# Kernel tuning notes

Hardware: AMD Instinct MI355X
Metric: run time of the kernel (lower is better)

## Reference

```python
import jax, jax.numpy as jnp
import numpy as np

EMBED = 1024
HEADS = 16
HEAD_DIM = EMBED // HEADS


def setup_inputs() -> dict:
    key = jax.random.key(0)
    ks = jax.random.split(key, 12)
    B, S = 2, 2048
    inp = {
        "query": jax.random.normal(ks[0], (B, S, EMBED), dtype=jnp.float32),
        "key": jax.random.normal(ks[1], (B, S, EMBED), dtype=jnp.float32),
        "value": jax.random.normal(ks[2], (B, S, EMBED), dtype=jnp.float32),
        "mask": jnp.ones((B, 1, 1, S), dtype=jnp.int32),
    }
    scale = 1.0 / np.sqrt(EMBED)
    inp["Wq"] = jax.random.normal(ks[3], (EMBED, EMBED), dtype=jnp.float32) * scale
    inp["bq"] = jax.random.normal(ks[4], (EMBED,), dtype=jnp.float32) * 0.01
    inp["Wk"] = jax.random.normal(ks[5], (EMBED, EMBED), dtype=jnp.float32) * scale
    inp["bk"] = jax.random.normal(ks[6], (EMBED,), dtype=jnp.float32) * 0.01
    inp["Wv"] = jax.random.normal(ks[7], (EMBED, EMBED), dtype=jnp.float32) * scale
    inp["bv"] = jax.random.normal(ks[8], (EMBED,), dtype=jnp.float32) * 0.01
    inp["Wo"] = jax.random.normal(ks[9], (EMBED, EMBED), dtype=jnp.float32) * scale
    inp["bo"] = jax.random.normal(ks[10], (EMBED,), dtype=jnp.float32) * 0.01
    return inp


def reference(query, key, value, mask, Wq, bq, Wk, bk, Wv, bv, Wo, bo):
    N, Lq, _ = query.shape
    Lk = key.shape[1]
    # Linear projections (torch Linear: x @ W.T + b)
    q = (query @ Wq.T + bq).reshape(N, Lq, HEADS, HEAD_DIM)
    k = (key @ Wk.T + bk).reshape(N, Lk, HEADS, HEAD_DIM)
    v = (value @ Wv.T + bv).reshape(N, Lk, HEADS, HEAD_DIM)
    # scores: [N, H, Lq, Lk]
    energy = jnp.einsum("nqhd,nkhd->nhqk", q, k)
    energy = jnp.where(mask == 0, jnp.float32(-1e20), energy)
    # NOTE: original scales by sqrt(embedSize), not sqrt(head_dim)
    attn = jax.nn.softmax(energy / jnp.sqrt(jnp.float32(EMBED)), axis=3)
    out = jnp.einsum("nhqv,nvhd->nqhd", attn, v).reshape(N, Lq, EMBED)
    return out @ Wo.T + bo
```

## Files before the change

### kernel.cpp

```cpp
#include <hip/hip_runtime.h>
#include <stdint.h>

typedef unsigned short u16;
typedef __attribute__((ext_vector_type(8))) short short8;
typedef __attribute__((ext_vector_type(4))) short short4v;
typedef __attribute__((ext_vector_type(4))) float floatx4;

#define AS_GLOBAL __attribute__((address_space(1)))
#define AS_LDS    __attribute__((address_space(3)))

#define QSCALE 0.045084220f

__device__ __forceinline__ float bf2f(u16 u) {
  union { unsigned int i; float f; } x; x.i = ((unsigned int)u) << 16; return x.f;
}
__device__ __forceinline__ u16 f2bf(float f) {
  union { float f; unsigned int i; } x; x.f = f;
  unsigned int u = x.i;
  u += 0x7fffu + ((u >> 16) & 1u);
  return (u16)(u >> 16);
}
__device__ __forceinline__ u16 f2bf_fast(float f) {
  union { float f; unsigned int i; } x; x.f = f;
  return (u16)((x.i + 0x8000u) >> 16);
}

__device__ __forceinline__ int probe_is_f32(const void* p) {
  const unsigned int* w = (const unsigned int*)p;
  int cnt = 0;
#pragma unroll
  for (int i = 0; i < 64; ++i) {
    unsigned int lo = w[i] & 0xFFFFu;
    int e = (int)((lo >> 7) & 0xFFu);
    cnt += (e >= 117 && e <= 137) ? 1 : 0;
  }
  return cnt < 32;
}

__device__ __forceinline__ short8 ld8(const void* P, size_t off, int isf32) {
  if (isf32) {
    const float* q = (const float*)P + off;
    float4 x = *(const float4*)q;
    float4 y = *(const float4*)(q + 4);
    short8 r;
    r[0] = (short)f2bf(x.x); r[1] = (short)f2bf(x.y);
    r[2] = (short)f2bf(x.z); r[3] = (short)f2bf(x.w);
    r[4] = (short)f2bf(y.x); r[5] = (short)f2bf(y.y);
    r[6] = (short)f2bf(y.z); r[7] = (short)f2bf(y.w);
    return r;
  }
  return *(const short8*)((const u16*)P + off);
}

__device__ __forceinline__ float ldscalar(const void* P, size_t idx, int isf32) {
  return isf32 ? ((const float*)P)[idx] : bf2f(((const u16*)P)[idx]);
}

__global__ __launch_bounds__(256) void cvt7(
    const void* s0, const void* s1, const void* s2, const void* s3,
    const void* s4, const void* s5, const void* s6,
    u16* d0, u16* d1, u16* d2, u16* d3, u16* d4, u16* d5, u16* d6)
{
  const int z = blockIdx.y;
  const void* src; u16* dst; int n;
  switch (z) {
    case 0: src = s0; dst = d0; n = 4194304; break;
    case 1: src = s1; dst = d1; n = 4194304; break;
    case 2: src = s2; dst = d2; n = 4194304; break;
    case 3: src = s3; dst = d3; n = 1048576; break;
    case 4: src = s4; dst = d4; n = 1048576; break;
    case 5: src = s5; dst = d5; n = 1048576; break;
    default: src = s6; dst = d6; n = 1048576; break;
  }
  const int isf32 = probe_is_f32(src);
  for (int i = blockIdx.x * 256 + threadIdx.x; i * 4 < n; i += gridDim.x * 256) {
    if (isf32) {
      float4 x = ((const float4*)src)[i];
      short4v r;
      r[0] = (short)f2bf(x.x); r[1] = (short)f2bf(x.y);
      r[2] = (short)f2bf(x.z); r[3] = (short)f2bf(x.w);
      *(short4v*)(dst + (size_t)i * 4) = r;
    } else {
      *(short4v*)(dst + (size_t)i * 4) = ((const short4v*)src)[i];
    }
  }
}

__device__ __forceinline__ void gemm_core_bf16(
    const u16* __restrict__ A, const u16* __restrict__ W,
    u16* As, u16* Bs, floatx4 acc[4][4], int m0, int n0, int K, int tid)
{
  const int lane = tid & 63, wv = tid >> 6;
  const int wm = wv >> 1, wn = wv & 1;
  const int g = lane >> 4, ml = lane & 15;
  const int r0 = tid >> 2, kc = (tid & 3) << 3;
  const u16* Ag0 = A + (size_t)(m0 + r0) * K + kc;
  const u16* Ag1 = A + (size_t)(m0 + r0 + 64) * K + kc;
  const u16* Bg0 = W + (size_t)(n0 + r0) * K + kc;
  const u16* Bg1 = W + (size_t)(n0 + r0 + 64) * K + kc;

#define STAGE_QKV(buf_, kt_) do {                                              \
    u16* a0 = As + (buf_) * 4096 + tid * 8;                                    \
    u16* b0 = Bs + (buf_) * 4096 + tid * 8;                                    \
    __builtin_amdgcn_global_load_lds((const AS_GLOBAL unsigned int*)(Ag0 + (kt_)), \
                                     (AS_LDS unsigned int*)a0, 16, 0, 0);      \
    __builtin_amdgcn_global_load_lds((const AS_GLOBAL unsigned int*)(Ag1 + (kt_)), \
                                     (AS_LDS unsigned int*)(a0 + 2048), 16, 0, 0); \
    __builtin_amdgcn_global_load_lds((const AS_GLOBAL unsigned int*)(Bg0 + (kt_)), \
                                     (AS_LDS unsigned int*)b0, 16, 0, 0);      \
    __builtin_amdgcn_global_load_lds((const AS_GLOBAL unsigned int*)(Bg1 + (kt_)), \
                                     (AS_LDS unsigned int*)(b0 + 2048), 16, 0, 0); \
  } while (0)

  STAGE_QKV(0, 0);
  int buf = 0;
#pragma unroll 2
  for (int kt = 0; kt < K; kt += 32) {
    const int nk = (kt + 32 < K) ? (kt + 32) : 0;
    STAGE_QKV(buf ^ 1, nk);
    __asm__ __volatile__("s_waitcnt vmcnt(4)\n\ts_barrier" ::: "memory");
    const u16* Ac = As + buf * 4096;
    const u16* Bc = Bs + buf * 4096;
    short8 af[4], bf[4];
#pragma unroll
    for (int i = 0; i < 4; ++i)
      af[i] = *(const short8*)(Ac + (wm * 64 + i * 16 + ml) * 32 + g * 8);
#pragma unroll
    for (int j = 0; j < 4; ++j)
      bf[j] = *(const short8*)(Bc + (wn * 64 + j * 16 + ml) * 32 + g * 8);
#pragma unroll
    for (int i = 0; i < 4; ++i)
#pragma unroll
      for (int j = 0; j < 4; ++j)
        acc[i][j] = __builtin_amdgcn_mfma_f32_16x16x32_bf16(af[i], bf[j], acc[i][j], 0, 0, 0);
    __asm__ __volatile__("s_waitcnt lgkmcnt(0)\n\ts_barrier" ::: "memory");
    buf ^= 1;
  }
#undef STAGE_QKV
  __asm__ __volatile__("s_waitcnt vmcnt(0)" ::: "memory");
}

__device__ __forceinline__ void gemm_core_cvt(
    const void* __restrict__ A, const void* __restrict__ W, int aF32, int bF32,
    u16* As, u16* Bs, floatx4 acc[4][4], int m0, int n0, int K, int tid)
{
  const int lane = tid & 63, wv = tid >> 6;
  const int wm = wv >> 1, wn = wv & 1;
  const int g = lane >> 4, ml = lane & 15;
  const int r0 = tid >> 2, kc = (tid & 3) << 3;
  const size_t offA0 = (size_t)(m0 + r0) * K + kc;
  const size_t offA1 = (size_t)(m0 + r0 + 64) * K + kc;
  const size_t offB0 = (size_t)(n0 + r0) * K + kc;
  const size_t offB1 = (size_t)(n0 + r0 + 64) * K + kc;
  u16* Al0 = As + tid * 8;  u16* Al1 = As + (tid + 256) * 8;
  u16* Bl0 = Bs + tid * 8;  u16* Bl1 = Bs + (tid + 256) * 8;
  for (int kt = 0; kt < K; kt += 32) {
    short8 a0 = ld8(A, offA0 + kt, aF32);
    short8 a1 = ld8(A, offA1 + kt, aF32);
    short8 b0 = ld8(W, offB0 + kt, bF32);
    short8 b1 = ld8(W, offB1 + kt, bF32);
    *(short8*)Al0 = a0;  *(short8*)Al1 = a1;
    *(short8*)Bl0 = b0;  *(short8*)Bl1 = b1;
    __syncthreads();
    short8 af[4], bf[4];
#pragma unroll
    for (int i = 0; i < 4; ++i)
      af[i] = *(const short8*)(As + (wm * 64 + i * 16 + ml) * 32 + g * 8);
#pragma unroll
    for (int j = 0; j < 4; ++j)
      bf[j] = *(const short8*)(Bs + (wn * 64 + j * 16 + ml) * 32 + g * 8);
#pragma unroll
    for (int i = 0; i < 4; ++i)
#pragma unroll
      for (int j = 0; j < 4; ++j)
        acc[i][j] = __builtin_amdgcn_mfma_f32_16x16x32_bf16(af[i], bf[j], acc[i][j], 0, 0, 0);
    __syncthreads();
  }
}

__device__ __forceinline__ void qkv_epilogue(
    floatx4 acc[4][4], const void* Bi, int cF32, u16* O, int m0, int n0,
    int tid, int z)
{
  const int lane = tid & 63, wv = tid >> 6;
  const int wm = wv >> 1, wn = wv & 1, g = lane >> 4, ml = lane & 15;
  const float sc = (z == 0) ? QSCALE : 1.0f;
#pragma unroll
  for (int j = 0; j < 4; ++j) {
    int gn = n0 + wn * 64 + j * 16 + ml;
    float bvv = ldscalar(Bi, (size_t)gn, cF32);
    int h = gn >> 6, d = gn & 63;
    if (z == 2) {
#pragma unroll
      for (int i = 0; i < 4; ++i) {
        int gm0 = m0 + wm * 64 + i * 16 + g * 4;
        int b = gm0 >> 11, s0 = gm0 & 2047;
        short4v pk;
#pragma unroll
        for (int r = 0; r < 4; ++r) pk[r] = (short)f2bf_fast(acc[i][j][r] + bvv);
        *(short4v*)(O + ((((size_t)b * 16 + h) * 64 + d) * 2048 + s0)) = pk;
      }
    } else {
#pragma unroll
      for (int i = 0; i < 4; ++i)
#pragma unroll
        for (int r = 0; r < 4; ++r) {
          int gm = m0 + wm * 64 + i * 16 + g * 4 + r;
          int b = gm >> 11, s = gm & 2047;
          O[(((size_t)b * 16 + h) * 2048 + s) * 64 + d] =
              f2bf_fast((acc[i][j][r] + bvv) * sc);
        }
    }
  }
}

__global__ __launch_bounds__(256) void qkv_gemm_bf16(
    const u16* __restrict__ Xq, const u16* __restrict__ Xk, const u16* __restrict__ Xv,
    const u16* __restrict__ Wq, const u16* __restrict__ Wk, const u16* __restrict__ Wv,
    const void* __restrict__ Bq, const void* __restrict__ Bk, const void* __restrict__ Bv,
    u16* __restrict__ Oq, u16* __restrict__ Ok, u16* __restrict__ Ov)
{
  __align__(16) __shared__ u16 As[8192];
  __align__(16) __shared__ u16 Bs[8192];
  const int z = blockIdx.z;
  const u16* X = (z == 0) ? Xq : (z == 1) ? Xk : Xv;
  const u16* W = (z == 0) ? Wq : (z == 1) ? Wk : Wv;
  const void* Bi = (z == 0) ? Bq : (z == 1) ? Bk : Bv;
  u16* O = (z == 0) ? Oq : (z == 1) ? Ok : Ov;
  const int tid = threadIdx.x;
  const int m0 = blockIdx.x * 128, n0 = blockIdx.y * 128;
  floatx4 acc[4][4] = {};
  gemm_core_bf16(X, W, As, Bs, acc, m0, n0, 1024, tid);
  const int cF32 = probe_is_f32(Bi);
  qkv_epilogue(acc, Bi, cF32, O, m0, n0, tid, z);
}

__global__ __launch_bounds__(256) void qkv_gemm_cvt(
    const void* __restrict__ Xq, const void* __restrict__ Xk, const void* __restrict__ Xv,
    const void* __restrict__ Wq, const void* __restrict__ Wk, const void* __restrict__ Wv,
    const void* __restrict__ Bq, const void* __restrict__ Bk, const void* __restrict__ Bv,
    u16* __restrict__ Oq, u16* __restrict__ Ok, u16* __restrict__ Ov)
{
  __align__(16) __shared__ u16 As[4096];
  __align__(16) __shared__ u16 Bs[4096];
  const int z = blockIdx.z;
  const void* X  = (z == 0) ? Xq : (z == 1) ? Xk : Xv;
  const void* W  = (z == 0) ? Wq : (z == 1) ? Wk : Wv;
  const void* Bi = (z == 0) ? Bq : (z == 1) ? Bk : Bv;
  u16* O = (z == 0) ? Oq : (z == 1) ? Ok : Ov;
  const int aF32 = probe_is_f32(X);
  const int bF32 = probe_is_f32(W);
  const int cF32 = probe_is_f32(Bi);
  const int tid = threadIdx.x;
  const int m0 = blockIdx.y * 128, n0 = blockIdx.x * 128;
  floatx4 acc[4][4] = {};
  gemm_core_cvt(X, W, aF32, bF32, As, Bs, acc, m0, n0, 1024, tid);
  qkv_epilogue(acc, Bi, cF32, O, m0, n0, tid, z);
}

__global__ __launch_bounds__(256) void out_gemm_bf16(
    const u16* __restrict__ X, const u16* __restrict__ W,
    const void* __restrict__ Bi, float* __restrict__ O)
{
  __align__(16) __shared__ u16 As[8192];
  __align__(16) __shared__ u16 Bs[8192];
  const int tid = threadIdx.x;
  const int m0 = blockIdx.x * 128, n0 = blockIdx.y * 128;
  floatx4 acc[4][4] = {};
  gemm_core_bf16(X, W, As, Bs, acc, m0, n0, 1024, tid);
  const int cF32 = probe_is_f32(Bi);
  const int lane = tid & 63, wv = tid >> 6;
  const int wm = wv >> 1, wn = wv & 1, g = lane >> 4, ml = lane & 15;
#pragma unroll
  for (int j = 0; j < 4; ++j) {
    int gn = n0 + wn * 64 + j * 16 + ml;
    float bvv = ldscalar(Bi, (size_t)gn, cF32);
#pragma unroll
    for (int i = 0; i < 4; ++i)
#pragma unroll
      for (int r = 0; r < 4; ++r) {
        int gm = m0 + wm * 64 + i * 16 + g * 4 + r;
        O[(size_t)gm * 1024 + gn] = acc[i][j][r] + bvv;
      }
  }
}

__global__ __launch_bounds__(256) void out_gemm_cvt(
    const u16* __restrict__ X, const void* __restrict__ W,
    const void* __restrict__ Bi, float* __restrict__ O)
{
  __align__(16) __shared__ u16 As[4096];
  __align__(16) __shared__ u16 Bs[4096];
  const int bF32 = probe_is_f32(W);
  const int cF32 = probe_is_f32(Bi);
  const int tid = threadIdx.x;
  const int m0 = blockIdx.y * 128, n0 = blockIdx.x * 128;
  floatx4 acc[4][4] = {};
  gemm_core_cvt(X, W, 0, bF32, As, Bs, acc, m0, n0, 1024, tid);
  const int lane = tid & 63, wv = tid >> 6;
  const int wm = wv >> 1, wn = wv & 1, g = lane >> 4, ml = lane & 15;
#pragma unroll
  for (int j = 0; j < 4; ++j) {
    int gn = n0 + wn * 64 + j * 16 + ml;
    float bvv = ldscalar(Bi, (size_t)gn, cF32);
#pragma unroll
    for (int i = 0; i < 4; ++i)
#pragma unroll
      for (int r = 0; r < 4; ++r) {
        int gm = m0 + wm * 64 + i * 16 + g * 4 + r;
        O[(size_t)gm * 1024 + gn] = acc[i][j][r] + bvv;
      }
  }
}

__global__ __launch_bounds__(256) void flash_attn(
    const u16* __restrict__ Q, const u16* __restrict__ K, const u16* __restrict__ V,
    const int* __restrict__ Mask, u16* __restrict__ O)
{
  __align__(16) __shared__ u16 Ks[2][4096];
  __align__(16) __shared__ u16 Vt[2][4096];
  __align__(16) __shared__ u16 Ps[4][16 * 72];
  __align__(16) __shared__ int Ms[64];
  __shared__ int Wok[4];

  const int qt2 = blockIdx.x;
  const int bh = blockIdx.y;
  const int b = bh >> 4, h = bh & 15;
  const int tid = threadIdx.x;
  const int lane = tid & 63, wv = tid >> 6;
  const int g = lane >> 4, ml = lane & 15;

  const size_t baseQ  = (((size_t)b * 16 + h) * 2048 + (size_t)qt2 * 128) * 64;
  const size_t baseKV = ((size_t)b * 16 + h) * 2048 * 64;

  {
    int la = 1;
#pragma unroll
    for (int i = 0; i < 8; ++i) la &= Mask[b * 2048 + tid * 8 + i];
    int wall = __all(la != 0);
    if (lane == 0) Wok[wv] = wall;
  }

  short8 qf[2][2];
#pragma unroll
  for (int u = 0; u < 2; ++u)
#pragma unroll
    for (int ks = 0; ks < 2; ++ks)
      qf[u][ks] = *(const short8*)(Q + baseQ +
          (size_t)(u * 64 + wv * 16 + ml) * 64 + ks * 32 + g * 8);

  const u16* kg[2]; const u16* vg[2];
#pragma unroll
  for (int t = 0; t < 2; ++t) {
    int s = tid + t * 256;
    int krow = s >> 3, kch = (s & 7) ^ (krow & 7);
    kg[t] = K + baseKV + (size_t)krow * 64 + kch * 8;
    int vd = s >> 3,  vch = (s & 7) ^ (vd & 7);
    vg[t] = V + baseKV + (size_t)vd * 2048 + vch * 8;
  }

  __syncthreads();
  const bool maskall = Wok[0] && Wok[1] && Wok[2] && Wok[3];

#define STAGE_FA(buf_) do {                                                    \
    u16* kb_ = Ks[buf_] + (size_t)(tid & 448) * 8;                             \
    u16* vb_ = Vt[buf_] + (size_t)(tid & 448) * 8;                             \
    __builtin_amdgcn_global_load_lds((const AS_GLOBAL unsigned int*)kg[0],     \
                                     (AS_LDS unsigned int*)kb_, 16, 0, 0);     \
    __builtin_amdgcn_global_load_lds((const AS_GLOBAL unsigned int*)kg[1],     \
                                     (AS_LDS unsigned int*)(kb_ + 2048), 16, 0, 0); \
    __builtin_amdgcn_global_load_lds((const AS_GLOBAL unsigned int*)vg[0],     \
                                     (AS_LDS unsigned int*)vb_, 16, 0, 0);     \
    __builtin_amdgcn_global_load_lds((const AS_GLOBAL unsigned int*)vg[1],     \
                                     (AS_LDS unsigned int*)(vb_ + 2048), 16, 0, 0); \
    kg[0] += 4096; kg[1] += 4096; vg[0] += 64; vg[1] += 64;                    \
  } while (0)

  floatx4 oacc[2][4] = {};
  float lp[2][4] = {};

  STAGE_FA(0);
  int buf = 0;
  for (int kv0 = 0; kv0 < 2048; kv0 += 64) {
    STAGE_FA(buf ^ 1);
    __asm__ __volatile__("s_waitcnt vmcnt(4)\n\ts_barrier" ::: "memory");
    if (!maskall && tid < 64) Ms[tid] = Mask[b * 2048 + kv0 + tid];
    const u16* Kc = Ks[buf];
    const u16* Vc = Vt[buf];

#pragma unroll
    for (int u = 0; u < 2; ++u) {
      float sv[4][4];
#pragma unroll
      for (int j = 0; j < 4; ++j) {
        floatx4 a = {0.f, 0.f, 0.f, 0.f};
        int row = j * 16 + ml;
#pragma unroll
        for (int ks = 0; ks < 2; ++ks) {
          short8 kb = *(const short8*)(Kc + row * 64 + ((((ks << 2) + g) ^ (row & 7)) << 3));
          a = __builtin_amdgcn_mfma_f32_16x16x32_bf16(qf[u][ks], kb, a, 0, 0, 0);
        }
#pragma unroll
        for (int r = 0; r < 4; ++r) sv[j][r] = a[r];
      }
      if (!maskall) {
        int mok[4];
#pragma unroll
        for (int j = 0; j < 4; ++j) mok[j] = Ms[j * 16 + ml];
#pragma unroll
        for (int j = 0; j < 4; ++j)
#pragma unroll
          for (int r = 0; r < 4; ++r)
            sv[j][r] = (mok[j] == 0) ? -1.0e30f : sv[j][r];
      }
#pragma unroll
      for (int j = 0; j < 4; ++j)
#pragma unroll
        for (int r = 0; r < 4; ++r) {
          float p = __builtin_amdgcn_exp2f(sv[j][r]);
          sv[j][r] = p;
          lp[u][r] += p;
        }
#pragma unroll
      for (int j = 0; j < 4; ++j)
#pragma unroll
        for (int r = 0; r < 4; ++r)
          Ps[wv][(g * 4 + r) * 72 + j * 16 + ml] = f2bf_fast(sv[j][r]);

      __asm__ __volatile__("s_waitcnt lgkmcnt(0)" ::: "memory");

      short8 pa[2];
#pragma unroll
      for (int j2 = 0; j2 < 2; ++j2)
        pa[j2] = *(const short8*)(&Ps[wv][ml * 72 + j2 * 32 + g * 8]);
#pragma unroll
      for (int t = 0; t < 4; ++t)
#pragma unroll
        for (int j2 = 0; j2 < 2; ++j2) {
          short8 vb = *(const short8*)(Vc + (t * 16 + ml) * 64 + ((((j2 << 2) + g) ^ (ml & 7)) << 3));
          oacc[u][t] = __builtin_amdgcn_mfma_f32_16x16x32_bf16(pa[j2], vb, oacc[u][t], 0, 0, 0);
        }
    }
    __asm__ __volatile__("s_waitcnt lgkmcnt(0)\n\ts_barrier" ::: "memory");
    buf ^= 1;
  }
#undef STAGE_FA
  __asm__ __volatile__("s_waitcnt vmcnt(0)" ::: "memory");

#pragma unroll
  for (int u = 0; u < 2; ++u) {
    float inv[4];
#pragma unroll
    for (int r = 0; r < 4; ++r) {
      float l = lp[u][r];
      l += __shfl_xor(l, 1);
      l += __shfl_xor(l, 2);
      l += __shfl_xor(l, 4);
      l += __shfl_xor(l, 8);
      inv[r] = (l > 0.f) ? 1.0f / l : 0.f;
    }
#pragma unroll
    for (int t = 0; t < 4; ++t)
#pragma unroll
      for (int r = 0; r < 4; ++r) {
        int q = qt2 * 128 + u * 64 + wv * 16 + g * 4 + r;
        int d = t * 16 + ml;
        O[((size_t)b * 2048 + q) * 1024 + h * 64 + d] = f2bf_fast(oacc[u][t][r] * inv[r]);
      }
  }
}

extern "C" void kernel_launch(void* const* d_in, const int* in_sizes, int n_in,
                              void* d_out, int out_size, void* d_ws, size_t ws_size,
                              hipStream_t stream) {
  const void* q_in = d_in[0];
  const void* k_in = d_in[1];
  const void* v_in = d_in[2];
  const int* mask = (const int*)d_in[3];
  const void* Wq = d_in[4];  const void* bq = d_in[5];
  const void* Wk = d_in[6];  const void* bk = d_in[7];
  const void* Wv = d_in[8];  const void* bv = d_in[9];
  const void* Wo = d_in[10]; const void* bo = d_in[11];

  const size_t NTOK = (size_t)2 * 2048 * 1024;
  const size_t NW   = (size_t)1024 * 1024;

  if (ws_size >= (size_t)67108864) {
    u16* CXq = (u16*)d_ws;
    u16* CXk = CXq + NTOK;
    u16* CXv = CXk + NTOK;
    u16* CWq = CXv + NTOK;
    u16* CWk = CWq + NW;
    u16* CWv = CWk + NW;
    u16* CWo = CWv + NW;
    u16* Qp  = CWo + NW;
    u16* Kp  = Qp + NTOK;
    u16* Vp  = Kp + NTOK;
    u16* Ao  = Vp + NTOK;

    cvt7<<<dim3(1024, 7), 256, 0, stream>>>(q_in, k_in, v_in, Wq, Wk, Wv, Wo,
                                            CXq, CXk, CXv, CWq, CWk, CWv, CWo);
    qkv_gemm_bf16<<<dim3(32, 8, 3), 256, 0, stream>>>(CXq, CXk, CXv,
                                                      CWq, CWk, CWv,
                                                      bq, bk, bv, Qp, Kp, Vp);
    flash_attn<<<dim3(16, 32), 256, 0, stream>>>(Qp, Kp, Vp, mask, Ao);
    out_gemm_bf16<<<dim3(32, 8), 256, 0, stream>>>(Ao, CWo, bo, (float*)d_out);
  } else {
    u16* Qp = (u16*)d_ws;
    u16* Kp = Qp + NTOK;
    u16* Vp = Kp + NTOK;
    u16* Ao = Vp + NTOK;

    qkv_gemm_cvt<<<dim3(8, 32, 3), 256, 0, stream>>>(q_in, k_in, v_in,
                                                     Wq, Wk, Wv, bq, bk, bv,
                                                     Qp, Kp, Vp);
    flash_attn<<<dim3(16, 32), 256, 0, stream>>>(Qp, Kp, Vp, mask, Ao);
    out_gemm_cvt<<<dim3(8, 32), 256, 0, stream>>>(Ao, Wo, bo, (float*)d_out);
  }
}
```

Measured before the change: 260.0 us.

## Fuse fp32-to-bf16 conversion into register-prefetched GEMM loads, drop separate convert pass

Removes the standalone conversion kernel that wrote bf16 copies of activations and weights to workspace. The GEMMs now load fp32 directly and convert in registers, with the next K-tile prefetched into registers while the current tile is computed. It uses a single LDS buffer and templated dtype paths. This saves a full read-and-write pass over about 28 MB of data and one launch. In exchange, GEMM loads double in width and the async global-to-LDS double buffering is lost.

```diff
diff --git a/kernel.cpp b/kernel.cpp
--- a/kernel.cpp
+++ b/kernel.cpp
@@ -56,126 +56,80 @@
   return isf32 ? ((const float*)P)[idx] : bf2f(((const u16*)P)[idx]);
 }
 
-__global__ __launch_bounds__(256) void cvt7(
-    const void* s0, const void* s1, const void* s2, const void* s3,
-    const void* s4, const void* s5, const void* s6,
-    u16* d0, u16* d1, u16* d2, u16* d3, u16* d4, u16* d5, u16* d6)
-{
-  const int z = blockIdx.y;
-  const void* src; u16* dst; int n;
-  switch (z) {
-    case 0: src = s0; dst = d0; n = 4194304; break;
-    case 1: src = s1; dst = d1; n = 4194304; break;
-    case 2: src = s2; dst = d2; n = 4194304; break;
-    case 3: src = s3; dst = d3; n = 1048576; break;
-    case 4: src = s4; dst = d4; n = 1048576; break;
-    case 5: src = s5; dst = d5; n = 1048576; break;
-    default: src = s6; dst = d6; n = 1048576; break;
-  }
-  const int isf32 = probe_is_f32(src);
-  for (int i = blockIdx.x * 256 + threadIdx.x; i * 4 < n; i += gridDim.x * 256) {
-    if (isf32) {
-      float4 x = ((const float4*)src)[i];
-      short4v r;
-      r[0] = (short)f2bf(x.x); r[1] = (short)f2bf(x.y);
-      r[2] = (short)f2bf(x.z); r[3] = (short)f2bf(x.w);
-      *(short4v*)(dst + (size_t)i * 4) = r;
-    } else {
-      *(short4v*)(dst + (size_t)i * 4) = ((const short4v*)src)[i];
-    }
-  }
-}
-
-__device__ __forceinline__ void gemm_core_bf16(
-    const u16* __restrict__ A, const u16* __restrict__ W,
+__device__ __forceinline__ short8 cvt8(float4 x, float4 y) {
+  short8 r;
+  r[0] = (short)f2bf_fast(x.x); r[1] = (short)f2bf_fast(x.y);
+  r[2] = (short)f2bf_fast(x.z); r[3] = (short)f2bf_fast(x.w);
+  r[4] = (short)f2bf_fast(y.x); r[5] = (short)f2bf_fast(y.y);
+  r[6] = (short)f2bf_fast(y.z); r[7] = (short)f2bf_fast(y.w);
+  return r;
+}
+
+template <int AF, int BF>
+__device__ __forceinline__ void gemm_pipe(
+    const void* __restrict__ A, const void* __restrict__ W,
     u16* As, u16* Bs, floatx4 acc[4][4], int m0, int n0, int K, int tid)
 {
   const int lane = tid & 63, wv = tid >> 6;
   const int wm = wv >> 1, wn = wv & 1;
   const int g = lane >> 4, ml = lane & 15;
   const int r0 = tid >> 2, kc = (tid & 3) << 3;
-  const u16* Ag0 = A + (size_t)(m0 + r0) * K + kc;
-  const u16* Ag1 = A + (size_t)(m0 + r0 + 64) * K + kc;
-  const u16* Bg0 = W + (size_t)(n0 + r0) * K + kc;
-  const u16* Bg1 = W + (size_t)(n0 + r0 + 64) * K + kc;
-
-#define STAGE_QKV(buf_, kt_) do {                                              \
-    u16* a0 = As + (buf_) * 4096 + tid * 8;                                    \
-    u16* b0 = Bs + (buf_) * 4096 + tid * 8;                                    \
-    __builtin_amdgcn_global_load_lds((const AS_GLOBAL unsigned int*)(Ag0 + (kt_)), \
-                                     (AS_LDS unsigned int*)a0, 16, 0, 0);      \
-    __builtin_amdgcn_global_load_lds((const AS_GLOBAL unsigned int*)(Ag1 + (kt_)), \
-                                     (AS_LDS unsigned int*)(a0 + 2048), 16, 0, 0); \
-    __builtin_amdgcn_global_load_lds((const AS_GLOBAL unsigned int*)(Bg0 + (kt_)), \
-                                     (AS_LDS unsigned int*)b0, 16, 0, 0);      \
-    __builtin_amdgcn_global_load_lds((const AS_GLOBAL unsigned int*)(Bg1 + (kt_)), \
-                                     (AS_LDS unsigned int*)(b0 + 2048), 16, 0, 0); \
+  const size_t oA0 = (size_t)(m0 + r0) * K + kc;
+  const size_t oA1 = (size_t)(m0 + r0 + 64) * K + kc;
+  const size_t oB0 = (size_t)(n0 + r0) * K + kc;
+  const size_t oB1 = (size_t)(n0 + r0 + 64) * K + kc;
+  u16* Al0 = As + tid * 8;  u16* Al1 = As + (tid + 256) * 8;
+  u16* Bl0 = Bs + tid * 8;  u16* Bl1 = Bs + (tid + 256) * 8;
+
+  float4 fa0[2], fa1[2], fb0[2], fb1[2];
+  short8 sa0, sa1, sb0, sb1;
+
+#define LOADT(kt_) do {                                                        \
+    if (AF) {                                                                  \
+      const float* p0 = (const float*)A + oA0 + (kt_);                         \
+      fa0[0] = ((const float4*)p0)[0]; fa0[1] = ((const float4*)p0)[1];        \
+      const float* p1 = (const float*)A + oA1 + (kt_);                         \
+      fa1[0] = ((const float4*)p1)[0]; fa1[1] = ((const float4*)p1)[1];        \
+    } else {                                                                   \
+      sa0 = *(const short8*)((const u16*)A + oA0 + (kt_));                     \
+      sa1 = *(const short8*)((const u16*)A + oA1 + (kt_));                     \
+    }                                                                          \
+    if (BF) {                                                                  \
+      const float* q0 = (const float*)W + oB0 + (kt_);                         \
+      fb0[0] = ((const float4*)q0)[0]; fb0[1] = ((const float4*)q0)[1];        \
+      const float* q1 = (const float*)W + oB1 + (kt_);                         \
+      fb1[0] = ((const float4*)q1)[0]; fb1[1] = ((const float4*)q1)[1];        \
+    } else {                                                                   \
+      sb0 = *(const short8*)((const u16*)W + oB0 + (kt_));                     \
+      sb1 = *(const short8*)((const u16*)W + oB1 + (kt_));                     \
+    }                                                                          \
   } while (0)
 
-  STAGE_QKV(0, 0);
-  int buf = 0;
-#pragma unroll 2
+  LOADT(0);
   for (int kt = 0; kt < K; kt += 32) {
-    const int nk = (kt + 32 < K) ? (kt + 32) : 0;
-    STAGE_QKV(buf ^ 1, nk);
-    __asm__ __volatile__("s_waitcnt vmcnt(4)\n\ts_barrier" ::: "memory");
-    const u16* Ac = As + buf * 4096;
-    const u16* Bc = Bs + buf * 4096;
+    __asm__ __volatile__("s_waitcnt lgkmcnt(0)\n\ts_barrier" ::: "memory");
+    *(short8*)Al0 = AF ? cvt8(fa0[0], fa0[1]) : sa0;
+    *(short8*)Al1 = AF ? cvt8(fa1[0], fa1[1]) : sa1;
+    *(short8*)Bl0 = BF ? cvt8(fb0[0], fb0[1]) : sb0;
+    *(short8*)Bl1 = BF ? cvt8(fb1[0], fb1[1]) : sb1;
+    const int nk = (kt + 32 < K) ? kt + 32 : 0;
+    LOADT(nk);
+    __asm__ __volatile__("s_waitcnt lgkmcnt(0)\n\ts_barrier" ::: "memory");
     short8 af[4], bf[4];
 #pragma unroll
     for (int i = 0; i < 4; ++i)
-      af[i] = *(const short8*)(Ac + (wm * 64 + i * 16 + ml) * 32 + g * 8);
+      af[i] = *(const short8*)(As + (wm * 64 + i * 16 + ml) * 32 + g * 8);
 #pragma unroll
     for (int j = 0; j < 4; ++j)
-      bf[j] = *(const short8*)(Bc + (wn * 64 + j * 16 + ml) * 32 + g * 8);
+      bf[j] = *(const short8*)(Bs + (wn * 64 + j * 16 + ml) * 32 + g * 8);
 #pragma unroll
     for (int i = 0; i < 4; ++i)
 #pragma unroll
       for (int j = 0; j < 4; ++j)
         acc[i][j] = __builtin_amdgcn_mfma_f32_16x16x32_bf16(af[i], bf[j], acc[i][j], 0, 0, 0);
-    __asm__ __volatile__("s_waitcnt lgkmcnt(0)\n\ts_barrier" ::: "memory");
-    buf ^= 1;
-  }
-#undef STAGE_QKV
+  }
+#undef LOADT
   __asm__ __volatile__("s_waitcnt vmcnt(0)" ::: "memory");
-}
-
-__device__ __forceinline__ void gemm_core_cvt(
-    const void* __restrict__ A, const void* __restrict__ W, int aF32, int bF32,
-    u16* As, u16* Bs, floatx4 acc[4][4], int m0, int n0, int K, int tid)
-{
-  const int lane = tid & 63, wv = tid >> 6;
-  const int wm = wv >> 1, wn = wv & 1;
-  const int g = lane >> 4, ml = lane & 15;
-  const int r0 = tid >> 2, kc = (tid & 3) << 3;
-  const size_t offA0 = (size_t)(m0 + r0) * K + kc;
-  const size_t offA1 = (size_t)(m0 + r0 + 64) * K + kc;
-  const size_t offB0 = (size_t)(n0 + r0) * K + kc;
-  const size_t offB1 = (size_t)(n0 + r0 + 64) * K + kc;
-  u16* Al0 = As + tid * 8;  u16* Al1 = As + (tid + 256) * 8;
-  u16* Bl0 = Bs + tid * 8;  u16* Bl1 = Bs + (tid + 256) * 8;
-  for (int kt = 0; kt < K; kt += 32) {
-    short8 a0 = ld8(A, offA0 + kt, aF32);
-    short8 a1 = ld8(A, offA1 + kt, aF32);
-    short8 b0 = ld8(W, offB0 + kt, bF32);
-    short8 b1 = ld8(W, offB1 + kt, bF32);
-    *(short8*)Al0 = a0;  *(short8*)Al1 = a1;
-    *(short8*)Bl0 = b0;  *(short8*)Bl1 = b1;
-    __syncthreads();
-    short8 af[4], bf[4];
-#pragma unroll
-    for (int i = 0; i < 4; ++i)
-      af[i] = *(const short8*)(As + (wm * 64 + i * 16 + ml) * 32 + g * 8);
-#pragma unroll
-    for (int j = 0; j < 4; ++j)
-      bf[j] = *(const short8*)(Bs + (wn * 64 + j * 16 + ml) * 32 + g * 8);
-#pragma unroll
-    for (int i = 0; i < 4; ++i)
-#pragma unroll
-      for (int j = 0; j < 4; ++j)
-        acc[i][j] = __builtin_amdgcn_mfma_f32_16x16x32_bf16(af[i], bf[j], acc[i][j], 0, 0, 0);
-    __syncthreads();
-  }
 }
 
 __device__ __forceinline__ void qkv_epilogue(
@@ -214,28 +168,7 @@
   }
 }
 
-__global__ __launch_bounds__(256) void qkv_gemm_bf16(
-    const u16* __restrict__ Xq, const u16* __restrict__ Xk, const u16* __restrict__ Xv,
-    const u16* __restrict__ Wq, const u16* __restrict__ Wk, const u16* __restrict__ Wv,
-    const void* __restrict__ Bq, const void* __restrict__ Bk, const void* __restrict__ Bv,
-    u16* __restrict__ Oq, u16* __restrict__ Ok, u16* __restrict__ Ov)
-{
-  __align__(16) __shared__ u16 As[8192];
-  __align__(16) __shared__ u16 Bs[8192];
-  const int z = blockIdx.z;
-  const u16* X = (z == 0) ? Xq : (z == 1) ? Xk : Xv;
-  const u16* W = (z == 0) ? Wq : (z == 1) ? Wk : Wv;
-  const void* Bi = (z == 0) ? Bq : (z == 1) ? Bk : Bv;
-  u16* O = (z == 0) ? Oq : (z == 1) ? Ok : Ov;
-  const int tid = threadIdx.x;
-  const int m0 = blockIdx.x * 128, n0 = blockIdx.y * 128;
-  floatx4 acc[4][4] = {};
-  gemm_core_bf16(X, W, As, Bs, acc, m0, n0, 1024, tid);
-  const int cF32 = probe_is_f32(Bi);
-  qkv_epilogue(acc, Bi, cF32, O, m0, n0, tid, z);
-}
-
-__global__ __launch_bounds__(256) void qkv_gemm_cvt(
+__global__ __launch_bounds__(256) void qkv_gemm(
     const void* __restrict__ Xq, const void* __restrict__ Xk, const void* __restrict__ Xv,
     const void* __restrict__ Wq, const void* __restrict__ Wk, const void* __restrict__ Wv,
     const void* __restrict__ Bq, const void* __restrict__ Bk, const void* __restrict__ Bv,
@@ -252,40 +185,16 @@
   const int bF32 = probe_is_f32(W);
   const int cF32 = probe_is_f32(Bi);
   const int tid = threadIdx.x;
-  const int m0 = blockIdx.y * 128, n0 = blockIdx.x * 128;
-  floatx4 acc[4][4] = {};
-  gemm_core_cvt(X, W, aF32, bF32, As, Bs, acc, m0, n0, 1024, tid);
-  qkv_epilogue(acc, Bi, cF32, O, m0, n0, tid, z);
-}
-
-__global__ __launch_bounds__(256) void out_gemm_bf16(
-    const u16* __restrict__ X, const u16* __restrict__ W,
-    const void* __restrict__ Bi, float* __restrict__ O)
-{
-  __align__(16) __shared__ u16 As[8192];
-  __align__(16) __shared__ u16 Bs[8192];
-  const int tid = threadIdx.x;
   const int m0 = blockIdx.x * 128, n0 = blockIdx.y * 128;
   floatx4 acc[4][4] = {};
-  gemm_core_bf16(X, W, As, Bs, acc, m0, n0, 1024, tid);
-  const int cF32 = probe_is_f32(Bi);
-  const int lane = tid & 63, wv = tid >> 6;
-  const int wm = wv >> 1, wn = wv & 1, g = lane >> 4, ml = lane & 15;
-#pragma unroll
-  for (int j = 0; j < 4; ++j) {
-    int gn = n0 + wn * 64 + j * 16 + ml;
-    float bvv = ldscalar(Bi, (size_t)gn, cF32);
-#pragma unroll
-    for (int i = 0; i < 4; ++i)
-#pragma unroll
-      for (int r = 0; r < 4; ++r) {
-        int gm = m0 + wm * 64 + i * 16 + g * 4 + r;
-        O[(size_t)gm * 1024 + gn] = acc[i][j][r] + bvv;
-      }
-  }
-}
-
-__global__ __launch_bounds__(256) void out_gemm_cvt(
+  if (aF32 && bF32)       gemm_pipe<1, 1>(X, W, As, Bs, acc, m0, n0, 1024, tid);
+  else if (!aF32 && !bF32) gemm_pipe<0, 0>(X, W, As, Bs, acc, m0, n0, 1024, tid);
+  else if (aF32)          gemm_pipe<1, 0>(X, W, As, Bs, acc, m0, n0, 1024, tid);
+  else                    gemm_pipe<0, 1>(X, W, As, Bs, acc, m0, n0, 1024, tid);
+  qkv_epilogue(acc, Bi, cF32, O, m0, n0, tid, z);
+}
+
+__global__ __launch_bounds__(256) void out_gemm(
     const u16* __restrict__ X, const void* __restrict__ W,
     const void* __restrict__ Bi, float* __restrict__ O)
 {
@@ -294,9 +203,10 @@
   const int bF32 = probe_is_f32(W);
   const int cF32 = probe_is_f32(Bi);
   const int tid = threadIdx.x;
-  const int m0 = blockIdx.y * 128, n0 = blockIdx.x * 128;
+  const int m0 = blockIdx.x * 128, n0 = blockIdx.y * 128;
   floatx4 acc[4][4] = {};
-  gemm_core_cvt(X, W, 0, bF32, As, Bs, acc, m0, n0, 1024, tid);
+  if (bF32) gemm_pipe<0, 1>(X, W, As, Bs, acc, m0, n0, 1024, tid);
+  else      gemm_pipe<0, 0>(X, W, As, Bs, acc, m0, n0, 1024, tid);
   const int lane = tid & 63, wv = tid >> 6;
   const int wm = wv >> 1, wn = wv & 1, g = lane >> 4, ml = lane & 15;
 #pragma unroll
@@ -483,38 +393,14 @@
   const void* Wo = d_in[10]; const void* bo = d_in[11];
 
   const size_t NTOK = (size_t)2 * 2048 * 1024;
-  const size_t NW   = (size_t)1024 * 1024;
-
-  if (ws_size >= (size_t)67108864) {
-    u16* CXq = (u16*)d_ws;
-    u16* CXk = CXq + NTOK;
-    u16* CXv = CXk + NTOK;
-    u16* CWq = CXv + NTOK;
-    u16* CWk = CWq + NW;
-    u16* CWv = CWk + NW;
-    u16* CWo = CWv + NW;
-    u16* Qp  = CWo + NW;
-    u16* Kp  = Qp + NTOK;
-    u16* Vp  = Kp + NTOK;
-    u16* Ao  = Vp + NTOK;
-
-    cvt7<<<dim3(1024, 7), 256, 0, stream>>>(q_in, k_in, v_in, Wq, Wk, Wv, Wo,
-                                            CXq, CXk, CXv, CWq, CWk, CWv, CWo);
-    qkv_gemm_bf16<<<dim3(32, 8, 3), 256, 0, stream>>>(CXq, CXk, CXv,
-                                                      CWq, CWk, CWv,
-                                                      bq, bk, bv, Qp, Kp, Vp);
-    flash_attn<<<dim3(16, 32), 256, 0, stream>>>(Qp, Kp, Vp, mask, Ao);
-    out_gemm_bf16<<<dim3(32, 8), 256, 0, stream>>>(Ao, CWo, bo, (float*)d_out);
-  } else {
-    u16* Qp = (u16*)d_ws;
-    u16* Kp = Qp + NTOK;
-    u16* Vp = Kp + NTOK;
-    u16* Ao = Vp + NTOK;
-
-    qkv_gemm_cvt<<<dim3(8, 32, 3), 256, 0, stream>>>(q_in, k_in, v_in,
-                                                     Wq, Wk, Wv, bq, bk, bv,
-                                                     Qp, Kp, Vp);
-    flash_attn<<<dim3(16, 32), 256, 0, stream>>>(Qp, Kp, Vp, mask, Ao);
-    out_gemm_cvt<<<dim3(8, 32), 256, 0, stream>>>(Ao, Wo, bo, (float*)d_out);
-  }
-}
+  u16* Qp = (u16*)d_ws;
+  u16* Kp = Qp + NTOK;
+  u16* Vp = Kp + NTOK;
+  u16* Ao = Vp + NTOK;
+
+  qkv_gemm<<<dim3(32, 8, 3), 256, 0, stream>>>(q_in, k_in, v_in,
+                                               Wq, Wk, Wv, bq, bk, bv,
+                                               Qp, Kp, Vp);
+  flash_attn<<<dim3(16, 32), 256, 0, stream>>>(Qp, Kp, Vp, mask, Ao);
+  out_gemm<<<dim3(32, 8), 256, 0, stream>>>(Ao, Wo, bo, (float*)d_out);
+}
```

Result: slower. 275.4 us (+5.9%).
